# Kernel tuning notes

Measured on AMD Instinct MI355X. Metric: run time of the kernel, lower is better.

## Reference

```python
import jax, jax.numpy as jnp
import numpy as np


def setup_inputs() -> dict:
    key = jax.random.key(0)
    k1, k2, k3 = jax.random.split(key, 3)
    num, c_in, c_out, din, dout = 64, 4, 4, 2, 2
    sx = sy = 256
    nx, ny = sx // 2 + sx % 2, sy // 2 + sy % 2
    x = jax.random.normal(k1, (num, c_in, din, sx, sy), dtype=jnp.float32)
    # weight tensor: (c_in, c_out, nx, ny, din, din, din, din, dout)
    tensors = jax.random.normal(k2, (c_in, c_out, nx, ny, din, din, din, din, dout), dtype=jnp.float32)
    bias = jax.random.normal(k3, (c_out, nx, ny, dout), dtype=jnp.float32) * 1e-8
    return {"x": x, "tensors": tensors, "bias": bias}


def reference(x, tensors, bias):
    # x: (n, c, d, sx, sy); tensors: (c, p, nx, ny, d, d, d, d, o); bias: (p, nx, ny, o)
    n, c, d, sx, sy = x.shape
    nx = sx // 2 + sx % 2
    ny = sy // 2 + sy % 2
    # boundary-clamped 2x2 patch indices (matches min(2*i+1, s-1) in the source)
    ix0 = jnp.arange(nx) * 2
    ix1 = jnp.minimum(ix0 + 1, sx - 1)
    iy0 = jnp.arange(ny) * 2
    iy1 = jnp.minimum(iy0 + 1, sy - 1)
    # four corner pixels of every 2x2 patch, each (n, c, d, nx, ny)
    a = x[:, :, :, ix0][:, :, :, :, iy0]  # (2i,   2j)
    b = x[:, :, :, ix1][:, :, :, :, iy0]  # (2i+1, 2j)
    e = x[:, :, :, ix0][:, :, :, :, iy1]  # (2i,   2j+1)
    f = x[:, :, :, ix1][:, :, :, :, iy1]  # (2i+1, 2j+1)
    # outer product of the four local features -> (n, c, nx, ny, d^4)
    patch = jnp.einsum('ncixy,ncjxy,nckxy,nclxy->ncxyijkl', a, b, e, f)
    patch = patch.reshape(n, c, nx, ny, d ** 4)
    c_out, dout = tensors.shape[1], tensors.shape[-1]
    w = tensors.reshape(c, c_out, nx, ny, d ** 4, dout)
    # per-position contraction over c_in and the d^4 patch index
    out = jnp.einsum('ncxyq,cpxyqo->npoxy', patch, w)
    out = out + bias.transpose(0, 3, 1, 2)[None]  # (1, p, o, nx, ny)
    return out
```

## Files before the change

### kernel.cpp

```cpp
#include <hip/hip_runtime.h>

#define NUMN 64
#define CIN 4
#define COUT 4
#define SX 256
#define SY 256
#define NXX 128
#define NYY 128
#define YTILE 32
#define NSPLIT 2
#define NPER (NUMN / NSPLIT)

__global__ __launch_bounds__(256, 2)
void ttn_kernel(const float* __restrict__ x, const float* __restrict__ w,
                const float* __restrict__ bias, float* __restrict__ out)
{
    __shared__ float lds[2][1024];

    const int bid = blockIdx.x;
    const int xi = bid % NXX;
    const int yt = (bid / NXX) % (NYY / YTILE);
    const int ns = bid / (NXX * (NYY / YTILE));

    const int tid = threadIdx.x;
    const int yl  = tid & (YTILE - 1);
    const int po  = tid >> 5;
    const int p   = po >> 1;
    const int o   = po & 1;
    const int y   = yt * YTILE + yl;

    float wr[CIN][16];
#pragma unroll
    for (int c = 0; c < CIN; ++c) {
        const float4* wp4 = (const float4*)(w +
            ((size_t)(((c * COUT + p) * NXX + xi) * NYY + y)) * 32);
#pragma unroll
        for (int j = 0; j < 8; ++j) {
            const float4 v = wp4[j];
            wr[c][2 * j]     = o ? v.y : v.x;
            wr[c][2 * j + 1] = o ? v.w : v.z;
        }
    }
    const float bv = bias[(((p * NXX + xi) * NYY + y) * 2) + o];

    const int mc   = tid >> 4;
    const int j0   = (tid & 15) * 4;
    const int prow = mc >> 1;
    const int r    = mc & 1;
    const size_t nstr = (size_t)CIN * 2 * SX * SY;
    const size_t ostr = (size_t)COUT * 2 * NXX * NYY;

    const float* xg = x + (size_t)(ns * NPER) * nstr
                        + ((size_t)prow * SX + (2 * xi + r)) * SY + yt * 64 + j0;
    float* ob = out + (size_t)(ns * NPER) * ostr
                    + (size_t)po * (NXX * NYY) + xi * NYY + y;
    float* ldsw = &lds[0][0] + tid * 4;

    float4 P0 = *(const float4*)xg;
    float4 P1 = *(const float4*)(xg + nstr);

    for (int n = 0; n < NPER; ++n) {
        const int cur = n & 1;
        *(float4*)(ldsw + cur * 1024) = P0;
        P0 = P1;
        const int np = (n + 2 < NPER) ? (n + 2) : (NPER - 1);
        P1 = *(const float4*)(xg + (size_t)np * nstr);

        __syncthreads();

        const float2* l2 = (const float2*)&lds[cur][0];
        float acc = bv;
#pragma unroll
        for (int c = 0; c < CIN; ++c) {
            const float2 ae0 = l2[c * 128 +       yl];
            const float2 bf0 = l2[c * 128 +  32 + yl];
            const float2 ae1 = l2[c * 128 +  64 + yl];
            const float2 bf1 = l2[c * 128 +  96 + yl];
            const float a0 = ae0.x, e0 = ae0.y, b0 = bf0.x, f0 = bf0.y;
            const float a1 = ae1.x, e1 = ae1.y, b1 = bf1.x, f1 = bf1.y;
            const float ef00 = e0*f0, ef01 = e0*f1, ef10 = e1*f0, ef11 = e1*f1;
            const float ab00 = a0*b0, ab01 = a0*b1, ab10 = a1*b0, ab11 = a1*b1;
            const float* wq = wr[c];
            float t;
            t = ef00*wq[ 0] + ef01*wq[ 1] + ef10*wq[ 2] + ef11*wq[ 3];  acc += ab00 * t;
            t = ef00*wq[ 4] + ef01*wq[ 5] + ef10*wq[ 6] + ef11*wq[ 7];  acc += ab01 * t;
            t = ef00*wq[ 8] + ef01*wq[ 9] + ef10*wq[10] + ef11*wq[11];  acc += ab10 * t;
            t = ef00*wq[12] + ef01*wq[13] + ef10*wq[14] + ef11*wq[15];  acc += ab11 * t;
        }
        ob[(size_t)n * ostr] = acc;
    }
}

extern "C" void kernel_launch(void* const* d_in, const int* in_sizes, int n_in,
                              void* d_out, int out_size, void* d_ws, size_t ws_size,
                              hipStream_t stream) {
    const float* x    = (const float*)d_in[0];
    const float* w    = (const float*)d_in[1];
    const float* bias = (const float*)d_in[2];
    float* out = (float*)d_out;

    const int grid = NXX * (NYY / YTILE) * NSPLIT;
    ttn_kernel<<<grid, 256, 0, stream>>>(x, w, bias, out);
}
```

Before: 238.7 us.

## Replace LDS staging with direct per-thread global float2 loads

Drops the shared-memory double buffer and the per-iteration __syncthreads. Each thread now loads its own 2x2 patch data straight from global memory as float2 reads. The goal is to remove barrier stalls and LDS traffic. The cost is that the 8 threads handling the same pixel (different p,o) issue redundant global loads that must be served from cache, and the explicit software prefetch of the next sample is lost.

After: 307.8 us. +29.0%, slower.

```diff
diff --git a/kernel.cpp b/kernel.cpp
--- a/kernel.cpp
+++ b/kernel.cpp
@@ -15,8 +15,6 @@
 void ttn_kernel(const float* __restrict__ x, const float* __restrict__ w,
                 const float* __restrict__ bias, float* __restrict__ out)
 {
-    __shared__ float lds[2][1024];
-
     const int bid = blockIdx.x;
     const int xi = bid % NXX;
     const int yt = (bid / NXX) % (NYY / YTILE);
@@ -43,41 +41,32 @@
     }
     const float bv = bias[(((p * NXX + xi) * NYY + y) * 2) + o];
 
-    const int mc   = tid >> 4;
-    const int j0   = (tid & 15) * 4;
-    const int prow = mc >> 1;
-    const int r    = mc & 1;
     const size_t nstr = (size_t)CIN * 2 * SX * SY;
     const size_t ostr = (size_t)COUT * 2 * NXX * NYY;
 
-    const float* xg = x + (size_t)(ns * NPER) * nstr
-                        + ((size_t)prow * SX + (2 * xi + r)) * SY + yt * 64 + j0;
+    const float* xp = x + (size_t)(ns * NPER) * nstr
+                        + (size_t)(2 * xi) * SY + 2 * y;
     float* ob = out + (size_t)(ns * NPER) * ostr
                     + (size_t)po * (NXX * NYY) + xi * NYY + y;
-    float* ldsw = &lds[0][0] + tid * 4;
-
-    float4 P0 = *(const float4*)xg;
-    float4 P1 = *(const float4*)(xg + nstr);
 
     for (int n = 0; n < NPER; ++n) {
-        const int cur = n & 1;
-        *(float4*)(ldsw + cur * 1024) = P0;
-        P0 = P1;
-        const int np = (n + 2 < NPER) ? (n + 2) : (NPER - 1);
-        P1 = *(const float4*)(xg + (size_t)np * nstr);
+        float2 ld[16];
+#pragma unroll
+        for (int c = 0; c < CIN; ++c) {
+            const float* pc = xp + (size_t)(2 * c) * (SX * SY);
+            ld[4 * c + 0] = *(const float2*)(pc);
+            ld[4 * c + 1] = *(const float2*)(pc + SY);
+            ld[4 * c + 2] = *(const float2*)(pc + SX * SY);
+            ld[4 * c + 3] = *(const float2*)(pc + SX * SY + SY);
+        }
 
-        __syncthreads();
-
-        const float2* l2 = (const float2*)&lds[cur][0];
         float acc = bv;
 #pragma unroll
         for (int c = 0; c < CIN; ++c) {
-            const float2 ae0 = l2[c * 128 +       yl];
-            const float2 bf0 = l2[c * 128 +  32 + yl];
-            const float2 ae1 = l2[c * 128 +  64 + yl];
-            const float2 bf1 = l2[c * 128 +  96 + yl];
-            const float a0 = ae0.x, e0 = ae0.y, b0 = bf0.x, f0 = bf0.y;
-            const float a1 = ae1.x, e1 = ae1.y, b1 = bf1.x, f1 = bf1.y;
+            const float a0 = ld[4 * c + 0].x, e0 = ld[4 * c + 0].y;
+            const float b0 = ld[4 * c + 1].x, f0 = ld[4 * c + 1].y;
+            const float a1 = ld[4 * c + 2].x, e1 = ld[4 * c + 2].y;
+            const float b1 = ld[4 * c + 3].x, f1 = ld[4 * c + 3].y;
             const float ef00 = e0*f0, ef01 = e0*f1, ef10 = e1*f0, ef11 = e1*f1;
             const float ab00 = a0*b0, ab01 = a0*b1, ab10 = a1*b0, ab11 = a1*b1;
             const float* wq = wr[c];
@@ -87,7 +76,9 @@
             t = ef00*wq[ 8] + ef01*wq[ 9] + ef10*wq[10] + ef11*wq[11];  acc += ab10 * t;
             t = ef00*wq[12] + ef01*wq[13] + ef10*wq[14] + ef11*wq[15];  acc += ab11 * t;
         }
-        ob[(size_t)n * ostr] = acc;
+        ob[0] = acc;
+        xp += nstr;
+        ob += ostr;
     }
 }
 
```
